# Kernel tuning notes

Hardware: AMD Instinct MI355X
Metric: run time of the kernel (lower is better)

Reference implementation:

```python
import jax, jax.numpy as jnp
import numpy as np


def _safe_sqrt(x):
    # cdist-style euclidean distance with grad-safe sqrt at 0
    return jnp.sqrt(jnp.maximum(x, 1e-12))


def setup_inputs() -> dict:
    key = jax.random.key(0)
    k1, k2, k3 = jax.random.split(key, 3)
    B, P, D, C, N = 256, 196, 768, 15, 12544
    return {
        "query_features": jax.random.normal(k1, (B, P, D), dtype=jnp.float32),
        "keys": jax.random.normal(k2, (C, P, D), dtype=jnp.float32),
        "embeddings": jax.random.normal(k3, (N, D), dtype=jnp.float32),
        "num_samples": 196,
    }


def _retrieve_key(query_features, keys):
    # torch.cdist(new_flat.unsqueeze(1), keys_flat.unsqueeze(0)).squeeze(1); min over classes
    B = query_features.shape[0]
    C = keys.shape[0]
    q = query_features.reshape(B, -1)  # [B, P*D]
    k = keys.reshape(C, -1)            # [C, P*D]
    sq = (jnp.sum(q * q, axis=1)[:, None]
          + jnp.sum(k * k, axis=1)[None, :]
          - 2.0 * (q @ k.T))           # [B, C] squared distances via GEMM
    d = _safe_sqrt(sq)
    min_dist = jnp.min(d, axis=1)
    min_idx = jnp.argmin(d, axis=1)
    return min_dist, min_idx


def _fps(embeddings, num_samples):
    # furthest_point_sampling_embeddings: iterative cdist-to-last-centroid,
    # running min of distances, argmax picks next centroid.
    # (torch version seeds with a random index; we use index 0 deterministically)
    N = embeddings.shape[0]
    sqn = jnp.sum(embeddings * embeddings, axis=1)  # [N]

    def step(carry, _):
        dists, last = carry
        c = embeddings[last]                          # [D]
        cur = _safe_sqrt(sqn - 2.0 * (embeddings @ c) + jnp.sum(c * c))
        dists = jnp.minimum(dists, cur)
        nxt = jnp.argmax(dists).astype(jnp.int32)
        return (dists, nxt), nxt

    init = (jnp.full((N,), jnp.inf, dtype=embeddings.dtype), jnp.int32(0))
    _, idxs = jax.lax.scan(step, init, None, length=num_samples - 1)
    idxs = jnp.concatenate([jnp.zeros((1,), dtype=idxs.dtype), idxs])
    return embeddings[idxs]  # [num_samples, D]


def reference(query_features, keys, embeddings, num_samples):
    min_dist, min_idx = _retrieve_key(query_features, keys)
    samples = _fps(embeddings, num_samples)
    return min_dist, min_idx, samples
```

## Files before the change

kernel.cpp:

```cpp
#include <hip/hip_runtime.h>
#include <math.h>

typedef unsigned long long u64;
typedef unsigned int u32;

#define L_TOT  150528
#define ROW4   37632
#define NCHUNK 7
#define CH4    5376
#define R_ITERS 84
#define NBT    32
#define BTILE  8
#define NCLS   15

#define N_E    12544
#define DIM    768
#define NBLK   256
#define PPB    49
#define NPPW   4
#define NSAMP  196
#define EPB    (PPB*DIM)

__device__ __forceinline__ float wave_sum(float v) {
#pragma unroll
  for (int m = 1; m < 64; m <<= 1) v += __shfl_xor(v, m, 64);
  return v;
}

__device__ __forceinline__ u64 wave_max_u64(u64 v) {
#pragma unroll
  for (int m = 1; m < 64; m <<= 1) {
    u64 o = __shfl_xor(v, m, 64);
    if (o > v) v = o;
  }
  return v;
}

__global__ __launch_bounds__(256) void retrieve_partial(
    const float* __restrict__ q, const float* __restrict__ k,
    float* __restrict__ part, float* __restrict__ kkpart) {
  const int bt = blockIdx.x;
  const int lc = blockIdx.y;
  const int tid = threadIdx.x;
  const int w = tid >> 6, lane = tid & 63;
  const int cbase = w * 4;
  const int ccnt = (w == 3) ? 3 : 4;
  const float4* qf = (const float4*)q;
  const float4* kf = (const float4*)k;
  const int fbase = lc * CH4 + lane;

  float acc[BTILE][4];
  float qq[BTILE];
  float kkv[4];
#pragma unroll
  for (int b = 0; b < BTILE; ++b) {
    qq[b] = 0.f;
#pragma unroll
    for (int c = 0; c < 4; ++c) acc[b][c] = 0.f;
  }
#pragma unroll
  for (int c = 0; c < 4; ++c) kkv[c] = 0.f;

  for (int it = 0; it < R_ITERS; ++it) {
    const int f = fbase + it * 64;
    float4 kv[4];
#pragma unroll
    for (int c = 0; c < 4; ++c)
      if (c < ccnt) kv[c] = kf[(size_t)(cbase + c) * ROW4 + f];
    if (bt == 0) {
#pragma unroll
      for (int c = 0; c < 4; ++c)
        if (c < ccnt)
          kkv[c] += kv[c].x*kv[c].x + kv[c].y*kv[c].y + kv[c].z*kv[c].z + kv[c].w*kv[c].w;
    }
#pragma unroll
    for (int b = 0; b < BTILE; ++b) {
      float4 qv = qf[(size_t)(bt * BTILE + b) * ROW4 + f];
#pragma unroll
      for (int c = 0; c < 4; ++c)
        if (c < ccnt)
          acc[b][c] += qv.x*kv[c].x + qv.y*kv[c].y + qv.z*kv[c].z + qv.w*kv[c].w;
      if (w == 3)
        qq[b] += qv.x*qv.x + qv.y*qv.y + qv.z*qv.z + qv.w*qv.w;
    }
  }

  const size_t pb = (size_t)(lc * NBT + bt) * 16;
#pragma unroll
  for (int b = 0; b < BTILE; ++b) {
#pragma unroll
    for (int c = 0; c < 4; ++c) {
      float v = wave_sum(acc[b][c]);
      if (lane == 0 && c < ccnt) part[(pb + cbase + c) * 8 + b] = v;
    }
    if (w == 3) {
      float v = wave_sum(qq[b]);
      if (lane == 0) part[(pb + 15) * 8 + b] = v;
    }
  }
  if (bt == 0) {
#pragma unroll
    for (int c = 0; c < 4; ++c) {
      float v = wave_sum(kkv[c]);
      if (lane == 0 && c < ccnt) kkpart[lc * 16 + cbase + c] = v;
    }
  }
}

__global__ __launch_bounds__(256) void retrieve_reduce(
    const float* __restrict__ part, const float* __restrict__ kkpart,
    float* __restrict__ out) {
  __shared__ float kn[NCLS];
  const int t = threadIdx.x;
  if (t < NCLS) {
    float s = 0.f;
    for (int lc = 0; lc < NCHUNK; ++lc) s += kkpart[lc * 16 + t];
    kn[t] = s;
  }
  __syncthreads();
  const int bt = t >> 3, bi = t & 7;
  float qq = 0.f;
  for (int lc = 0; lc < NCHUNK; ++lc)
    qq += part[((size_t)(lc * NBT + bt) * 16 + 15) * 8 + bi];
  float dmin = INFINITY;
  int didx = 0;
  for (int c = 0; c < NCLS; ++c) {
    float dot = 0.f;
    for (int lc = 0; lc < NCHUNK; ++lc)
      dot += part[((size_t)(lc * NBT + bt) * 16 + c) * 8 + bi];
    float d2 = qq + kn[c] - 2.f * dot;
    float d = sqrtf(fmaxf(d2, 1e-12f));
    if (d < dmin) { dmin = d; didx = c; }
  }
  out[t] = dmin;
  out[256 + t] = (float)didx;
}

__global__ __launch_bounds__(1024, 4) void fps_kernel(
    const float* __restrict__ emb,
    u64* __restrict__ words,
    u64* __restrict__ result,
    float* __restrict__ out_samples) {
  extern __shared__ float e_lds[];
  const int tid = threadIdx.x;
  const int blk = blockIdx.x;
  const int w = tid >> 6, lane = tid & 63;

  __shared__ int hist[NSAMP];
  __shared__ u64 wkey[16];
  __shared__ u64 swin[4];

  {
    const float* src = emb + (size_t)blk * EPB;
    for (int i = tid; i < EPB; i += 1024) e_lds[i] = src[i];
  }
  __syncthreads();

  float sq[NPPW];
  float dist2[NPPW];
#pragma unroll
  for (int i = 0; i < NPPW; ++i) {
    const int p = w + 16 * i;
    float s = 0.f;
    if (p < PPB) {
#pragma unroll
      for (int j = 0; j < 12; ++j) {
        float v = e_lds[p * DIM + lane + 64 * j];
        s += v * v;
      }
    }
    sq[i] = wave_sum(s);
    dist2[i] = INFINITY;
  }
  int last = 0;
  if (tid == 0) hist[0] = 0;
  __syncthreads();

  for (int s = 1; s < NSAMP; ++s) {
    const int buf = (s & 1) * NBLK;

    float c[12];
    float cn = 0.f;
    const size_t cb = (size_t)last * DIM;
#pragma unroll
    for (int j = 0; j < 12; ++j) {
      float v = emb[cb + lane + 64 * j];
      c[j] = v;
      cn += v * v;
    }
    cn = wave_sum(cn);

    u64 bk = 0ull;
#pragma unroll
    for (int i = 0; i < NPPW; ++i) {
      const int p = w + 16 * i;
      if (p < PPB) {
        float a = 0.f;
#pragma unroll
        for (int j = 0; j < 12; ++j) a = fmaf(e_lds[p * DIM + lane + 64 * j], c[j], a);
        a = wave_sum(a);
        float d2 = sq[i] - 2.f * a + cn;
        if (d2 < dist2[i]) dist2[i] = d2;
        u32 fb = __float_as_uint(dist2[i]);
        u64 key = ((u64)fb << 32) | (u32)(~(u32)(blk * PPB + p));
        if (key > bk) bk = key;
      }
    }
    if (lane == 0) wkey[w] = bk;
    __syncthreads();

    if (w == 0) {
      u64 k = wkey[lane & 15];
#pragma unroll
      for (int m = 1; m < 16; m <<= 1) {
        u64 o = __shfl_xor(k, m, 64);
        if (o > k) k = o;
      }
      if (lane == 0) {
        const u32 bidx = ~(u32)(k & 0xffffffffull);
        const u32 bdist = (u32)(k >> 32);
        const u64 word = ((u64)s << 48) | ((u64)bdist << 16) | (u64)bidx;
        __hip_atomic_store(&words[buf + blk], word, __ATOMIC_RELAXED,
                           __HIP_MEMORY_SCOPE_AGENT);
      }
    }

    if (blk == 0) {
      if (tid < NBLK) {
        u64 w64;
        for (;;) {
          w64 = __hip_atomic_load(&words[buf + tid], __ATOMIC_RELAXED,
                                  __HIP_MEMORY_SCOPE_AGENT);
          if ((w64 >> 48) >= (u64)s) break;
        }
        u64 kk = (((w64 >> 16) & 0xffffffffull) << 32) |
                 (u64)(u32)(~(u32)(w64 & 0xffffull));
        kk = wave_max_u64(kk);
        if (lane == 0) swin[w] = kk;
      }
      __syncthreads();
      if (tid == 0) {
        u64 m = swin[0];
#pragma unroll
        for (int qi = 1; qi < 4; ++qi) if (swin[qi] > m) m = swin[qi];
        const int widx = (int)(~(u32)(m & 0xffffffffull));
        hist[s] = widx;
        __hip_atomic_store(&result[s & 1], ((u64)s << 32) | (u32)widx,
                           __ATOMIC_RELAXED, __HIP_MEMORY_SCOPE_AGENT);
      }
      __syncthreads();
    } else {
      if (tid == 0) {
        u64 r;
        for (;;) {
          r = __hip_atomic_load(&result[s & 1], __ATOMIC_RELAXED,
                                __HIP_MEMORY_SCOPE_AGENT);
          if ((r >> 32) >= (u64)s) break;
        }
        hist[s] = (int)(u32)(r & 0xffffffffull);
      }
      __syncthreads();
    }
    last = hist[s];
  }

  if (blk < NSAMP) {
    const int idx = hist[blk];
    const float4* src = (const float4*)(emb + (size_t)idx * DIM);
    float4* dst = (float4*)(out_samples + (size_t)blk * DIM);
    if (tid < DIM / 4) dst[tid] = src[tid];
  }
}

extern "C" void kernel_launch(void* const* d_in, const int* in_sizes, int n_in,
                              void* d_out, int out_size, void* d_ws, size_t ws_size,
                              hipStream_t stream) {
  const float* q   = (const float*)d_in[0];
  const float* k   = (const float*)d_in[1];
  const float* emb = (const float*)d_in[2];
  float* out = (float*)d_out;

  u64* words  = (u64*)d_ws;
  u64* result = (u64*)((char*)d_ws + 4096);
  float* part   = (float*)((char*)d_ws + 8192);
  float* kkpart = part + 28672;

  hipMemsetAsync(d_ws, 0, 4096 + 16, stream);

  hipLaunchKernelGGL(retrieve_partial, dim3(NBT, NCHUNK), dim3(256), 0, stream,
                     q, k, part, kkpart);
  hipLaunchKernelGGL(retrieve_reduce, dim3(1), dim3(256), 0, stream,
                     part, kkpart, out);

  hipFuncSetAttribute((const void*)fps_kernel,
                      hipFuncAttributeMaxDynamicSharedMemorySize,
                      EPB * sizeof(float));

  float* samples = out + 512;
  void* args[] = {(void*)&emb, (void*)&words, (void*)&result, (void*)&samples};
  hipLaunchCooperativeKernel((void*)fps_kernel, dim3(NBLK), dim3(1024), args,
                             EPB * sizeof(float), stream);
}
```

Baseline: 879.3 us.

## Map four points per wave with 16-lane groups and unroll polling loads in FPS

The FPS kernel now assigns one point to each 16-lane quarter-wave, so each wave handles four points at once. Each lane uses float4 loads from LDS and global memory and reduces within the quarter-wave, replacing four sequential points per wave that each needed a full 64-lane reduction. This shortens the per-step dependent shuffle chains and gives the step loop more instruction-level parallelism. The spin-wait on the broadcast result now issues four atomic loads per loop iteration, which may cut poll latency but adds memory traffic.

```diff
diff --git a/kernel.cpp b/kernel.cpp
--- a/kernel.cpp
+++ b/kernel.cpp
@@ -17,7 +17,6 @@
 #define DIM    768
 #define NBLK   256
 #define PPB    49
-#define NPPW   4
 #define NSAMP  196
 #define EPB    (PPB*DIM)
 
@@ -145,6 +144,11 @@
   const int tid = threadIdx.x;
   const int blk = blockIdx.x;
   const int w = tid >> 6, lane = tid & 63;
+  const int q4 = lane >> 4;
+  const int r = lane & 15;
+  const int pl = w * 4 + q4;
+  const bool valid = pl < PPB;
+  const int p = valid ? pl : 0;
 
   __shared__ int hist[NSAMP];
   __shared__ u64 wkey[16];
@@ -156,22 +160,21 @@
   }
   __syncthreads();
 
-  float sq[NPPW];
-  float dist2[NPPW];
-#pragma unroll
-  for (int i = 0; i < NPPW; ++i) {
-    const int p = w + 16 * i;
-    float s = 0.f;
-    if (p < PPB) {
-#pragma unroll
-      for (int j = 0; j < 12; ++j) {
-        float v = e_lds[p * DIM + lane + 64 * j];
-        s += v * v;
-      }
-    }
-    sq[i] = wave_sum(s);
-    dist2[i] = INFINITY;
-  }
+  const float4* ef = (const float4*)(e_lds + (size_t)p * DIM);
+  float sq;
+  {
+    float ss = 0.f;
+#pragma unroll
+    for (int jj = 0; jj < 12; ++jj) {
+      float4 v = ef[r + jj * 16];
+      ss = fmaf(v.x, v.x, ss); ss = fmaf(v.y, v.y, ss);
+      ss = fmaf(v.z, v.z, ss); ss = fmaf(v.w, v.w, ss);
+    }
+#pragma unroll
+    for (int m = 1; m < 16; m <<= 1) ss += __shfl_xor(ss, m, 64);
+    sq = ss;
+  }
+  float dist2 = INFINITY;
   int last = 0;
   if (tid == 0) hist[0] = 0;
   __syncthreads();
@@ -179,34 +182,40 @@
   for (int s = 1; s < NSAMP; ++s) {
     const int buf = (s & 1) * NBLK;
 
-    float c[12];
-    float cn = 0.f;
-    const size_t cb = (size_t)last * DIM;
-#pragma unroll
-    for (int j = 0; j < 12; ++j) {
-      float v = emb[cb + lane + 64 * j];
-      c[j] = v;
-      cn += v * v;
-    }
-    cn = wave_sum(cn);
-
-    u64 bk = 0ull;
-#pragma unroll
-    for (int i = 0; i < NPPW; ++i) {
-      const int p = w + 16 * i;
-      if (p < PPB) {
-        float a = 0.f;
-#pragma unroll
-        for (int j = 0; j < 12; ++j) a = fmaf(e_lds[p * DIM + lane + 64 * j], c[j], a);
-        a = wave_sum(a);
-        float d2 = sq[i] - 2.f * a + cn;
-        if (d2 < dist2[i]) dist2[i] = d2;
-        u32 fb = __float_as_uint(dist2[i]);
-        u64 key = ((u64)fb << 32) | (u32)(~(u32)(blk * PPB + p));
-        if (key > bk) bk = key;
-      }
-    }
-    if (lane == 0) wkey[w] = bk;
+    const float4* cf = (const float4*)(emb + (size_t)last * DIM);
+    float4 cv[12];
+#pragma unroll
+    for (int jj = 0; jj < 12; ++jj) cv[jj] = cf[r + jj * 16];
+
+    float a = 0.f, cn = 0.f;
+#pragma unroll
+    for (int jj = 0; jj < 12; ++jj) {
+      float4 e4 = ef[r + jj * 16];
+      float4 c4 = cv[jj];
+      a = fmaf(e4.x, c4.x, a); a = fmaf(e4.y, c4.y, a);
+      a = fmaf(e4.z, c4.z, a); a = fmaf(e4.w, c4.w, a);
+      cn = fmaf(c4.x, c4.x, cn); cn = fmaf(c4.y, c4.y, cn);
+      cn = fmaf(c4.z, c4.z, cn); cn = fmaf(c4.w, c4.w, cn);
+    }
+#pragma unroll
+    for (int m = 1; m < 16; m <<= 1) {
+      a += __shfl_xor(a, m, 64);
+      cn += __shfl_xor(cn, m, 64);
+    }
+
+    u64 key = 0ull;
+    if (valid) {
+      float d2 = sq - 2.f * a + cn;
+      if (d2 < dist2) dist2 = d2;
+      key = ((u64)__float_as_uint(dist2) << 32) |
+            (u32)(~(u32)(blk * PPB + pl));
+    }
+#pragma unroll
+    for (int m = 16; m < 64; m <<= 1) {
+      u64 o = __shfl_xor(key, m, 64);
+      if (o > key) key = o;
+    }
+    if (lane == 0) wkey[w] = key;
     __syncthreads();
 
     if (w == 0) {
@@ -251,13 +260,22 @@
       __syncthreads();
     } else {
       if (tid == 0) {
-        u64 r;
+        u64 r0, r1, r2, r3, rr;
         for (;;) {
-          r = __hip_atomic_load(&result[s & 1], __ATOMIC_RELAXED,
-                                __HIP_MEMORY_SCOPE_AGENT);
-          if ((r >> 32) >= (u64)s) break;
+          r0 = __hip_atomic_load(&result[s & 1], __ATOMIC_RELAXED,
+                                 __HIP_MEMORY_SCOPE_AGENT);
+          r1 = __hip_atomic_load(&result[s & 1], __ATOMIC_RELAXED,
+                                 __HIP_MEMORY_SCOPE_AGENT);
+          r2 = __hip_atomic_load(&result[s & 1], __ATOMIC_RELAXED,
+                                 __HIP_MEMORY_SCOPE_AGENT);
+          r3 = __hip_atomic_load(&result[s & 1], __ATOMIC_RELAXED,
+                                 __HIP_MEMORY_SCOPE_AGENT);
+          if ((r3 >> 32) >= (u64)s) { rr = r3; break; }
+          if ((r2 >> 32) >= (u64)s) { rr = r2; break; }
+          if ((r1 >> 32) >= (u64)s) { rr = r1; break; }
+          if ((r0 >> 32) >= (u64)s) { rr = r0; break; }
         }
-        hist[s] = (int)(u32)(r & 0xffffffffull);
+        hist[s] = (int)(u32)(rr & 0xffffffffull);
       }
       __syncthreads();
     }
```

Result: slower. 902.5 us (+2.6%).
